# Kernel optimization log

Hardware: AMD Instinct MI355X
Metric: run time of the kernel (lower is better)

## Reference

```python
import jax, jax.numpy as jnp
import numpy as np

B, LQ, LK, DQ, DKEY, DV = 8, 2048, 2048, 1024, 1024, 1024
MASK_NEG = -1e6  # d2l masked_softmax fill value


def setup_inputs() -> dict:
    key = jax.random.key(0)
    kq, kk, kv, kl, kw = jax.random.split(key, 5)
    queries = jax.random.normal(kq, (B, LQ, DQ), dtype=jnp.float32)
    keys = jax.random.normal(kk, (B, LK, DKEY), dtype=jnp.float32)
    values = jax.random.normal(kv, (B, LK, DV), dtype=jnp.float32)
    valid_lens = jax.random.randint(kl, (B,), 1, LK + 1)
    W_q = jax.random.normal(kw, (DQ, DKEY), dtype=jnp.float32) / np.sqrt(DQ)
    return {"queries": queries, "keys": keys, "values": values,
            "valid_lens": valid_lens, "W_q": W_q}


def reference(queries, keys, values, valid_lens, W_q):
    # Q projection: LazyLinear(key_dim, bias=False)
    q = jnp.einsum("bqd,dk->bqk", queries, W_q)          # [B, LQ, DKEY]
    d = q.shape[-1]
    scores = jnp.einsum("bqk,bsk->bqs", q, keys) / jnp.sqrt(jnp.asarray(d, q.dtype))
    # masked_softmax: positions >= valid_len set to -1e6 before softmax
    mask = jnp.arange(scores.shape[-1])[None, None, :] < valid_lens[:, None, None]
    scores = jnp.where(mask, scores, MASK_NEG)
    attn = jax.nn.softmax(scores, axis=-1)               # [B, LQ, LK]
    # dropout p=0.0 (eval) -> identity
    return jnp.einsum("bqs,bsv->bqv", attn, values)      # [B, LQ, DV]
```

## Files before the change

### kernel.cpp

```cpp
#include <hip/hip_runtime.h>
#include <cstdint>
#include <cstddef>

#define B_   8
#define LQ_  2048
#define LK_  2048

typedef __attribute__((ext_vector_type(8))) __bf16 bf16x8;
typedef __attribute__((ext_vector_type(4))) float f32x4;
typedef __attribute__((ext_vector_type(8))) unsigned short ushortx8;

__device__ __forceinline__ unsigned short f2bf(float f) {
  unsigned u = __builtin_bit_cast(unsigned, f);
  u = u + 0x7fffu + ((u >> 16) & 1u);
  return (unsigned short)(u >> 16);
}
__device__ __forceinline__ float bf2f(unsigned short h) {
  unsigned u = ((unsigned)h) << 16;
  return __builtin_bit_cast(float, u);
}

__device__ __forceinline__ void gld_lds16(const void* g, void* l) {
  __builtin_amdgcn_global_load_lds((__attribute__((address_space(1))) void*)(void*)g,
                                   (__attribute__((address_space(3))) void*)l, 16, 0, 0);
}

__global__ __launch_bounds__(256) void cast3_bf16_kernel(
    const float* __restrict__ q, unsigned short* __restrict__ qo,
    const float* __restrict__ k, unsigned short* __restrict__ ko,
    const float* __restrict__ w, unsigned short* __restrict__ wo,
    const int* __restrict__ vlp) {
  int bb = (int)blockIdx.x;
  const float* in;
  unsigned short* out;
  if (bb < 8192) {
    in = q; out = qo;
  } else if (bb < 16384) {
    bb -= 8192;
    in = k; out = ko;
    int batch = bb >> 10;
    int row = (bb & 1023) * 2;
    int vl = vlp[batch];
    if (row >= ((vl + 127) & ~127)) return;
  } else {
    bb -= 16384;
    in = w; out = wo;
  }
  size_t i = ((size_t)bb * 256 + threadIdx.x) * 8;
  float4 a = *(const float4*)(in + i);
  float4 b = *(const float4*)(in + i + 4);
  ushortx8 o;
  o[0] = f2bf(a.x); o[1] = f2bf(a.y); o[2] = f2bf(a.z); o[3] = f2bf(a.w);
  o[4] = f2bf(b.x); o[5] = f2bf(b.y); o[6] = f2bf(b.z); o[7] = f2bf(b.w);
  *(ushortx8*)(out + i) = o;
}

__global__ __launch_bounds__(256) void transpose_cast_kernel(
    const float* __restrict__ in, unsigned short* __restrict__ out,
    int R, int C, long in_bstride, long out_bstride, const int* __restrict__ vlp) {
  __shared__ float t[32][33];
  int r0 = blockIdx.y * 32;
  if (vlp) {
    int kEnd = (vlp[blockIdx.z] + 63) & ~63;
    if (r0 >= kEnd) return;
  }
  const float* inb = in + (size_t)blockIdx.z * in_bstride;
  unsigned short* outb = out + (size_t)blockIdx.z * out_bstride;
  int c0 = blockIdx.x * 32;
  int tx = threadIdx.x, ty = threadIdx.y;
#pragma unroll
  for (int k = 0; k < 4; ++k) {
    int r = ty + k * 8;
    t[r][tx] = inb[(size_t)(r0 + r) * C + c0 + tx];
  }
  __syncthreads();
#pragma unroll
  for (int k = 0; k < 4; ++k) {
    int c = ty + k * 8;
    outb[(size_t)(c0 + c) * R + r0 + tx] = f2bf(t[tx][c]);
  }
}

template <int OUTM, int SKIPN, int SKIPM, int CLAMPK>
__global__ __launch_bounds__(256, 2) void gemm128_kernel(
    const unsigned short* __restrict__ A, const unsigned short* __restrict__ B,
    void* __restrict__ Cp, int M, int N, int K,
    long a_bstride, long b_bstride, long c_bstride, float scale,
    const int* __restrict__ vlp, int lognx) {
  __shared__ unsigned short lds[4][2][64 * 64];

  const int tid = threadIdx.x;
  const int wid = tid >> 6;
  const int lane = tid & 63;
  const int lane15 = lane & 15;
  const int lhalf = lane >> 4;

  const int idx = (int)blockIdx.x;
  const int z = idx & 7;
  const int rest = idx >> 3;
  const int nxm = (1 << lognx) - 1;
  const int xt = rest & nxm;
  const int yt = rest >> lognx;
  const int nt = (xt + 2 * z) & nxm;
  const int m0 = yt * 128;
  const int n0 = nt * 128;

  int vl = K;
  if constexpr (SKIPN || SKIPM || CLAMPK) vl = vlp[z];
  if constexpr (SKIPN) {
    if (n0 >= vl) return;
  }
  if constexpr (SKIPM) {
    if (m0 >= vl) return;
  }
  int kEnd = K;
  if constexpr (CLAMPK) {
    int ke = (vl + 63) & ~63;
    kEnd = ke < K ? ke : K;
  }
  const int nKt = kEnd >> 5;

  const unsigned short* Ab = A + (size_t)z * a_bstride;
  const unsigned short* Bb = B + (size_t)z * b_bstride;

  int srowA[2], srowB[2], scol[2], sdst[2];
#pragma unroll
  for (int j = 0; j < 2; ++j) {
    int blk = (wid * 2 + j) * 64 + lane;
    int p = blk >> 3, q = blk & 7;
    int c = q ^ (p & 7);
    int r = 2 * p + (c >> 2);
    scol[j] = (c & 3) * 8;
    srowA[j] = m0 + r;
    srowB[j] = n0 + r;
    sdst[j] = blk * 8;
  }

  const int om = (wid & 1) * 64;
  const int on = (wid >> 1) * 64;
  const int swz8 = ((((lane15 & 1) << 2) + lhalf) ^ ((lane15 >> 1) & 7)) << 3;
  const int aBase = ((om >> 1) + (lane15 >> 1)) * 64 + swz8;
  const int bBase = ((on >> 1) + (lane15 >> 1)) * 64 + swz8;

  f32x4 acc[4][4];
#pragma unroll
  for (int f = 0; f < 4; ++f)
#pragma unroll
    for (int g = 0; g < 4; ++g) acc[f][g] = (f32x4){0.f, 0.f, 0.f, 0.f};

#pragma unroll
  for (int j = 0; j < 2; ++j)
    gld_lds16(Ab + (size_t)srowA[j] * K + scol[j], &lds[0][0][sdst[j]]);
#pragma unroll
  for (int j = 0; j < 2; ++j)
    gld_lds16(Bb + (size_t)srowB[j] * K + scol[j], &lds[0][1][sdst[j]]);
#pragma unroll
  for (int j = 0; j < 2; ++j)
    gld_lds16(Ab + (size_t)srowA[j] * K + (32 + scol[j]), &lds[1][0][sdst[j]]);
#pragma unroll
  for (int j = 0; j < 2; ++j)
    gld_lds16(Bb + (size_t)srowB[j] * K + (32 + scol[j]), &lds[1][1][sdst[j]]);
  if (nKt > 2) {
#pragma unroll
    for (int j = 0; j < 2; ++j)
      gld_lds16(Ab + (size_t)srowA[j] * K + (64 + scol[j]), &lds[2][0][sdst[j]]);
#pragma unroll
    for (int j = 0; j < 2; ++j)
      gld_lds16(Bb + (size_t)srowB[j] * K + (64 + scol[j]), &lds[2][1][sdst[j]]);
    asm volatile("s_waitcnt vmcnt(8)" ::: "memory");
  } else {
    asm volatile("s_waitcnt vmcnt(4)" ::: "memory");
  }
  __builtin_amdgcn_s_barrier();

  for (int t = 0; t < nKt; ++t) {
    const unsigned short* lA = &lds[t & 3][0][0];
    const unsigned short* lB = &lds[t & 3][1][0];
    const bool st = (t + 3) < nKt;
    const int nb = (t + 3) & 3;
    const int kc = (t + 3) * 32;

    bf16x8 a[4], b[4];
#pragma unroll
    for (int f = 0; f < 4; ++f) a[f] = *(const bf16x8*)&lA[aBase + f * 512];
#pragma unroll
    for (int g = 0; g < 4; ++g) b[g] = *(const bf16x8*)&lB[bBase + g * 512];
    if (st) {
#pragma unroll
      for (int j = 0; j < 2; ++j)
        gld_lds16(Ab + (size_t)srowA[j] * K + (kc + scol[j]), &lds[nb][0][sdst[j]]);
#pragma unroll
      for (int j = 0; j < 2; ++j)
        gld_lds16(Bb + (size_t)srowB[j] * K + (kc + scol[j]), &lds[nb][1][sdst[j]]);
    }
    asm volatile("s_waitcnt lgkmcnt(0)" ::: "memory");
    __builtin_amdgcn_sched_barrier(0);
    __builtin_amdgcn_s_setprio(1);
#pragma unroll
    for (int f = 0; f < 4; ++f)
#pragma unroll
      for (int g = 0; g < 4; ++g)
        acc[f][g] = __builtin_amdgcn_mfma_f32_16x16x32_bf16(a[f], b[g], acc[f][g], 0, 0, 0);
    __builtin_amdgcn_s_setprio(0);
    {
      int hi = nKt < t + 4 ? nKt : t + 4;
      int pend = hi - (t + 2);
      if (pend >= 2)
        asm volatile("s_waitcnt vmcnt(8)" ::: "memory");
      else if (pend == 1)
        asm volatile("s_waitcnt vmcnt(4)" ::: "memory");
      else
        asm volatile("s_waitcnt vmcnt(0)" ::: "memory");
    }
    __builtin_amdgcn_s_barrier();
  }

  const size_t boffC = (size_t)z * c_bstride;
#pragma unroll
  for (int f = 0; f < 4; ++f) {
    int row = m0 + om + f * 16 + lhalf * 4;
#pragma unroll
    for (int g = 0; g < 4; ++g) {
      int col = n0 + on + g * 16 + lane15;
#pragma unroll
      for (int r = 0; r < 4; ++r) {
        float v = acc[f][g][r];
        if constexpr (OUTM == 0) {
          ((unsigned short*)Cp + boffC)[(size_t)(row + r) * N + col] = f2bf(v);
        } else if constexpr (OUTM == 1) {
          ((unsigned short*)Cp + boffC)[(size_t)(row + r) * N + col] = f2bf(v * scale);
        } else {
          ((float*)Cp + boffC)[(size_t)(row + r) * N + col] = v;
        }
      }
    }
  }
}

__global__ __launch_bounds__(256) void softmax_kernel(unsigned short* __restrict__ scores,
                                                      const int* __restrict__ valid_lens) {
  const int row = blockIdx.x;
  const int b = row >> 11;
  const int vl = valid_lens[b];
  const int kEnd = (vl + 63) & ~63;
  unsigned short* rp = scores + (size_t)row * LK_;
  const int tid = threadIdx.x;
  const int wid = tid >> 6, lane = tid & 63;
  __shared__ float sred[4];

  const int cb = tid * 8;
  const bool act = cb < kEnd;
  ushortx8 h = {};
  if (act) h = *(const ushortx8*)(rp + cb);
  float x[8];
#pragma unroll
  for (int t = 0; t < 8; ++t) x[t] = bf2f(h[t]);

  float m = -3.4e38f;
#pragma unroll
  for (int t = 0; t < 8; ++t)
    if (cb + t < vl) m = fmaxf(m, x[t]);
#pragma unroll
  for (int off = 32; off >= 1; off >>= 1) m = fmaxf(m, __shfl_xor(m, off));
  if (lane == 0) sred[wid] = m;
  __syncthreads();
  m = fmaxf(fmaxf(sred[0], sred[1]), fmaxf(sred[2], sred[3]));
  __syncthreads();

  float e[8];
  float s = 0.f;
#pragma unroll
  for (int t = 0; t < 8; ++t) {
    e[t] = (cb + t < vl) ? __expf(x[t] - m) : 0.f;
    s += e[t];
  }
#pragma unroll
  for (int off = 32; off >= 1; off >>= 1) s += __shfl_xor(s, off);
  if (lane == 0) sred[wid] = s;
  __syncthreads();
  s = sred[0] + sred[1] + sred[2] + sred[3];
  float inv = 1.f / s;

  if (act) {
    ushortx8 o;
#pragma unroll
    for (int t = 0; t < 8; ++t) o[t] = f2bf(e[t] * inv);
    *(ushortx8*)(rp + cb) = o;
  }
}

extern "C" void kernel_launch(void* const* d_in, const int* in_sizes, int n_in,
                              void* d_out, int out_size, void* d_ws, size_t ws_size,
                              hipStream_t stream) {
  const float* queries = (const float*)d_in[0];
  const float* keys = (const float*)d_in[1];
  const float* values = (const float*)d_in[2];
  const int* valid_lens = (const int*)d_in[3];
  const float* W_q = (const float*)d_in[4];
  float* out = (float*)d_out;

  unsigned short* ws = (unsigned short*)d_ws;
  const size_t M1 = (size_t)1024 * 1024;
  unsigned short* q_bf = ws;
  unsigned short* scores = ws + 16 * M1;
  unsigned short* keysP = ws + 48 * M1;
  unsigned short* valsT = keysP;
  unsigned short* w_bf = ws + 64 * M1;
  unsigned short* keys_bf = ws + 65 * M1;

  cast3_bf16_kernel<<<dim3(16896), 256, 0, stream>>>(
      queries, q_bf, keys, keys_bf, W_q, w_bf, valid_lens);
  gemm128_kernel<0, 0, 1, 0><<<dim3(16 * 8 * 8), 256, 0, stream>>>(
      keys_bf, w_bf, keysP, 2048, 1024, 1024,
      (long)2048 * 1024, 0, (long)2048 * 1024, 1.f, valid_lens, 3);
  gemm128_kernel<1, 1, 0, 0><<<dim3(16 * 16 * 8), 256, 0, stream>>>(
      q_bf, keysP, scores, 2048, 2048, 1024,
      (long)2048 * 1024, (long)2048 * 1024, (long)2048 * 2048, 0.03125f, valid_lens, 4);
  transpose_cast_kernel<<<dim3(32, 64, 8), dim3(32, 8), 0, stream>>>(
      values, valsT, 2048, 1024, (long)2048 * 1024, (long)1024 * 2048, valid_lens);
  softmax_kernel<<<dim3(B_ * LQ_), 256, 0, stream>>>(scores, valid_lens);
  gemm128_kernel<2, 0, 0, 1><<<dim3(16 * 8 * 8), 256, 0, stream>>>(
      scores, valsT, out, 2048, 1024, 2048,
      (long)2048 * 2048, (long)1024 * 2048, (long)2048 * 1024, 1.f, valid_lens, 3);
}
```

Baseline: 397.1 us.

## Enlarge GEMM tiles to 256x128 with three-stage LDS pipeline

Grows the GEMM block tile from 128x128 to 256x128, so each wave computes a 128x64 sub-tile with 32 MFMA accumulators. The aim is more reuse of each loaded B fragment and fewer LDS and global loads per FLOP. The LDS pipeline drops from four stages to three to stay within shared-memory limits, and the key cast skip is rounded to 256 rows to match the SKIPM granularity. The trade-offs are higher register pressure, fewer blocks in flight, shallower prefetch, and coarser skipping at valid_len boundaries.

```diff
diff --git a/kernel.cpp b/kernel.cpp
--- a/kernel.cpp
+++ b/kernel.cpp
@@ -41,7 +41,7 @@
     int batch = bb >> 10;
     int row = (bb & 1023) * 2;
     int vl = vlp[batch];
-    if (row >= ((vl + 127) & ~127)) return;
+    if (row >= ((vl + 255) & ~255)) return;
   } else {
     bb -= 16384;
     in = w; out = wo;
@@ -82,12 +82,12 @@
 }
 
 template <int OUTM, int SKIPN, int SKIPM, int CLAMPK>
-__global__ __launch_bounds__(256, 2) void gemm128_kernel(
+__global__ __launch_bounds__(256, 2) void gemm256x128_kernel(
     const unsigned short* __restrict__ A, const unsigned short* __restrict__ B,
     void* __restrict__ Cp, int M, int N, int K,
     long a_bstride, long b_bstride, long c_bstride, float scale,
     const int* __restrict__ vlp, int lognx) {
-  __shared__ unsigned short lds[4][2][64 * 64];
+  __shared__ unsigned short lds[3][128 * 64 + 64 * 64];
 
   const int tid = threadIdx.x;
   const int wid = tid >> 6;
@@ -102,7 +102,7 @@
   const int xt = rest & nxm;
   const int yt = rest >> lognx;
   const int nt = (xt + 2 * z) & nxm;
-  const int m0 = yt * 128;
+  const int m0 = yt * 256;
   const int n0 = nt * 128;
 
   int vl = K;
@@ -123,101 +123,88 @@
   const unsigned short* Ab = A + (size_t)z * a_bstride;
   const unsigned short* Bb = B + (size_t)z * b_bstride;
 
-  int srowA[2], srowB[2], scol[2], sdst[2];
+  int srA[4], scA[4], sdA[4];
+#pragma unroll
+  for (int j = 0; j < 4; ++j) {
+    int blk = (wid * 4 + j) * 64 + lane;
+    int p = blk >> 3;
+    int c = (blk & 7) ^ (p & 7);
+    srA[j] = m0 + 2 * p + (c >> 2);
+    scA[j] = (c & 3) * 8;
+    sdA[j] = blk * 8;
+  }
+  int srB[2], scB[2], sdB[2];
 #pragma unroll
   for (int j = 0; j < 2; ++j) {
     int blk = (wid * 2 + j) * 64 + lane;
-    int p = blk >> 3, q = blk & 7;
-    int c = q ^ (p & 7);
-    int r = 2 * p + (c >> 2);
-    scol[j] = (c & 3) * 8;
-    srowA[j] = m0 + r;
-    srowB[j] = n0 + r;
-    sdst[j] = blk * 8;
-  }
-
-  const int om = (wid & 1) * 64;
+    int p = blk >> 3;
+    int c = (blk & 7) ^ (p & 7);
+    srB[j] = n0 + 2 * p + (c >> 2);
+    scB[j] = (c & 3) * 8;
+    sdB[j] = 8192 + blk * 8;
+  }
+
+  const int om = (wid & 1) * 128;
   const int on = (wid >> 1) * 64;
   const int swz8 = ((((lane15 & 1) << 2) + lhalf) ^ ((lane15 >> 1) & 7)) << 3;
   const int aBase = ((om >> 1) + (lane15 >> 1)) * 64 + swz8;
-  const int bBase = ((on >> 1) + (lane15 >> 1)) * 64 + swz8;
-
-  f32x4 acc[4][4];
-#pragma unroll
-  for (int f = 0; f < 4; ++f)
+  const int bBase = 8192 + ((on >> 1) + (lane15 >> 1)) * 64 + swz8;
+
+  f32x4 acc[8][4];
+#pragma unroll
+  for (int f = 0; f < 8; ++f)
 #pragma unroll
     for (int g = 0; g < 4; ++g) acc[f][g] = (f32x4){0.f, 0.f, 0.f, 0.f};
 
-#pragma unroll
-  for (int j = 0; j < 2; ++j)
-    gld_lds16(Ab + (size_t)srowA[j] * K + scol[j], &lds[0][0][sdst[j]]);
-#pragma unroll
-  for (int j = 0; j < 2; ++j)
-    gld_lds16(Bb + (size_t)srowB[j] * K + scol[j], &lds[0][1][sdst[j]]);
-#pragma unroll
-  for (int j = 0; j < 2; ++j)
-    gld_lds16(Ab + (size_t)srowA[j] * K + (32 + scol[j]), &lds[1][0][sdst[j]]);
-#pragma unroll
-  for (int j = 0; j < 2; ++j)
-    gld_lds16(Bb + (size_t)srowB[j] * K + (32 + scol[j]), &lds[1][1][sdst[j]]);
-  if (nKt > 2) {
-#pragma unroll
-    for (int j = 0; j < 2; ++j)
-      gld_lds16(Ab + (size_t)srowA[j] * K + (64 + scol[j]), &lds[2][0][sdst[j]]);
-#pragma unroll
-    for (int j = 0; j < 2; ++j)
-      gld_lds16(Bb + (size_t)srowB[j] * K + (64 + scol[j]), &lds[2][1][sdst[j]]);
-    asm volatile("s_waitcnt vmcnt(8)" ::: "memory");
-  } else {
-    asm volatile("s_waitcnt vmcnt(4)" ::: "memory");
-  }
+#define STAGE_TILE(T, S)                                                        \
+  {                                                                             \
+    const int kc_ = (T) * 32;                                                   \
+    _Pragma("unroll")                                                           \
+    for (int j = 0; j < 4; ++j)                                                 \
+      gld_lds16(Ab + (size_t)srA[j] * K + (kc_ + scA[j]), &lds[S][sdA[j]]);     \
+    _Pragma("unroll")                                                           \
+    for (int j = 0; j < 2; ++j)                                                 \
+      gld_lds16(Bb + (size_t)srB[j] * K + (kc_ + scB[j]), &lds[S][sdB[j]]);     \
+  }
+
+  STAGE_TILE(0, 0);
+  STAGE_TILE(1, 1);
+  asm volatile("s_waitcnt vmcnt(6)" ::: "memory");
   __builtin_amdgcn_s_barrier();
 
+  int cs = 0;
   for (int t = 0; t < nKt; ++t) {
-    const unsigned short* lA = &lds[t & 3][0][0];
-    const unsigned short* lB = &lds[t & 3][1][0];
-    const bool st = (t + 3) < nKt;
-    const int nb = (t + 3) & 3;
-    const int kc = (t + 3) * 32;
-
-    bf16x8 a[4], b[4];
-#pragma unroll
-    for (int f = 0; f < 4; ++f) a[f] = *(const bf16x8*)&lA[aBase + f * 512];
-#pragma unroll
-    for (int g = 0; g < 4; ++g) b[g] = *(const bf16x8*)&lB[bBase + g * 512];
-    if (st) {
-#pragma unroll
-      for (int j = 0; j < 2; ++j)
-        gld_lds16(Ab + (size_t)srowA[j] * K + (kc + scol[j]), &lds[nb][0][sdst[j]]);
-#pragma unroll
-      for (int j = 0; j < 2; ++j)
-        gld_lds16(Bb + (size_t)srowB[j] * K + (kc + scol[j]), &lds[nb][1][sdst[j]]);
-    }
+    const unsigned short* lcur = &lds[cs][0];
+    const bool st = (t + 2) < nKt;
+    const int ss = cs == 0 ? 2 : cs - 1;
+
+    bf16x8 a[8], b[4];
+#pragma unroll
+    for (int f = 0; f < 8; ++f) a[f] = *(const bf16x8*)&lcur[aBase + f * 512];
+#pragma unroll
+    for (int g = 0; g < 4; ++g) b[g] = *(const bf16x8*)&lcur[bBase + g * 512];
+    if (st) STAGE_TILE(t + 2, ss);
     asm volatile("s_waitcnt lgkmcnt(0)" ::: "memory");
     __builtin_amdgcn_sched_barrier(0);
     __builtin_amdgcn_s_setprio(1);
 #pragma unroll
-    for (int f = 0; f < 4; ++f)
+    for (int f = 0; f < 8; ++f)
 #pragma unroll
       for (int g = 0; g < 4; ++g)
         acc[f][g] = __builtin_amdgcn_mfma_f32_16x16x32_bf16(a[f], b[g], acc[f][g], 0, 0, 0);
     __builtin_amdgcn_s_setprio(0);
-    {
-      int hi = nKt < t + 4 ? nKt : t + 4;
-      int pend = hi - (t + 2);
-      if (pend >= 2)
-        asm volatile("s_waitcnt vmcnt(8)" ::: "memory");
-      else if (pend == 1)
-        asm volatile("s_waitcnt vmcnt(4)" ::: "memory");
-      else
-        asm volatile("s_waitcnt vmcnt(0)" ::: "memory");
-    }
+    if (st)
+      asm volatile("s_waitcnt vmcnt(6)" ::: "memory");
+    else
+      asm volatile("s_waitcnt vmcnt(0)" ::: "memory");
     __builtin_amdgcn_s_barrier();
-  }
+    cs = cs == 2 ? 0 : cs + 1;
+  }
+#undef STAGE_TILE
 
   const size_t boffC = (size_t)z * c_bstride;
 #pragma unroll
-  for (int f = 0; f < 4; ++f) {
+  for (int f = 0; f < 8; ++f) {
     int row = m0 + om + f * 16 + lhalf * 4;
 #pragma unroll
     for (int g = 0; g < 4; ++g) {
@@ -310,16 +297,16 @@
 
   cast3_bf16_kernel<<<dim3(16896), 256, 0, stream>>>(
       queries, q_bf, keys, keys_bf, W_q, w_bf, valid_lens);
-  gemm128_kernel<0, 0, 1, 0><<<dim3(16 * 8 * 8), 256, 0, stream>>>(
+  gemm256x128_kernel<0, 0, 1, 0><<<dim3(8 * 8 * 8), 256, 0, stream>>>(
       keys_bf, w_bf, keysP, 2048, 1024, 1024,
       (long)2048 * 1024, 0, (long)2048 * 1024, 1.f, valid_lens, 3);
-  gemm128_kernel<1, 1, 0, 0><<<dim3(16 * 16 * 8), 256, 0, stream>>>(
+  gemm256x128_kernel<1, 1, 0, 0><<<dim3(8 * 16 * 8), 256, 0, stream>>>(
       q_bf, keysP, scores, 2048, 2048, 1024,
       (long)2048 * 1024, (long)2048 * 1024, (long)2048 * 2048, 0.03125f, valid_lens, 4);
   transpose_cast_kernel<<<dim3(32, 64, 8), dim3(32, 8), 0, stream>>>(
       values, valsT, 2048, 1024, (long)2048 * 1024, (long)1024 * 2048, valid_lens);
   softmax_kernel<<<dim3(B_ * LQ_), 256, 0, stream>>>(scores, valid_lens);
-  gemm128_kernel<2, 0, 0, 1><<<dim3(16 * 8 * 8), 256, 0, stream>>>(
+  gemm256x128_kernel<2, 0, 0, 1><<<dim3(8 * 8 * 8), 256, 0, stream>>>(
       scores, valsT, out, 2048, 1024, 2048,
       (long)2048 * 2048, (long)1024 * 2048, (long)2048 * 1024, 1.f, valid_lens, 3);
 }
```

Result: faster. 374.8 us (-5.6%).
